# Kernel tuning notes

Hardware: AMD Instinct MI355X
Metric: run time of the kernel (lower is better)

Reference implementation:

```python
import jax, jax.numpy as jnp
import numpy as np

WS = 8          # window size
HEADS = 3       # num_heads
DIM = 48        # channels


def _rel_pos_log(ws):
    # log-spaced relative coordinates, (N, N, 2) with N = ws*ws
    coords = jnp.stack(jnp.meshgrid(jnp.arange(ws), jnp.arange(ws), indexing='ij'))  # (2, ws, ws)
    cf = coords.reshape(2, -1)                                  # (2, N)
    rel = (cf[:, :, None] - cf[:, None, :]).transpose(1, 2, 0)  # (N, N, 2)
    rel = rel.astype(jnp.float32)
    return jnp.sign(rel) * jnp.log1p(jnp.abs(rel))


def setup_inputs() -> dict:
    key = jax.random.key(0)
    ks = jax.random.split(key, 11)
    s = 0.05  # keep pre-softmax logits in a sane range
    return {
        'X': jax.random.normal(ks[0], (2, DIM, 512, 512), jnp.float32),
        'v_w': jax.random.normal(ks[1], (DIM, DIM), jnp.float32) * s,
        'v_b': jnp.zeros((DIM,), jnp.float32),
        'qk_w': jax.random.normal(ks[2], (2 * DIM, DIM), jnp.float32) * s,
        'qk_b': jnp.zeros((2 * DIM,), jnp.float32),
        'proj_w': jax.random.normal(ks[3], (DIM, DIM), jnp.float32) * s,
        'proj_b': jnp.zeros((DIM,), jnp.float32),
        'meta1_w': jax.random.normal(ks[4], (256, 2), jnp.float32) * s,
        'meta1_b': jnp.zeros((256,), jnp.float32),
        'meta2_w': jax.random.normal(ks[5], (HEADS, 256), jnp.float32) * s,
        'meta2_b': jnp.zeros((HEADS,), jnp.float32),
    }


def _conv1x1(x, w, b):
    # x: [B, Cin, H, W], w: [Cout, Cin], b: [Cout]
    return jnp.einsum('oc,bchw->bohw', w, x) + b[None, :, None, None]


def reference(X, v_w, v_b, qk_w, qk_b, proj_w, proj_b,
              meta1_w, meta1_b, meta2_w, meta2_b):
    B, C, H, W = X.shape
    hd = C // HEADS
    scale = hd ** -0.5
    N = WS * WS

    V = _conv1x1(X, v_w, v_b)              # [B, C, H, W]
    QK = _conv1x1(X, qk_w, qk_b)           # [B, 2C, H, W]
    QKV = jnp.concatenate([QK, V], axis=1)  # [B, 3C, H, W]

    # window partition (shift=0, H/W multiples of WS -> no padding)
    nh, nw = H // WS, W // WS
    x = QKV.transpose(0, 2, 3, 1)                           # [B, H, W, 3C]
    x = x.reshape(B, nh, WS, nw, WS, 3 * C)
    x = x.transpose(0, 1, 3, 2, 4, 5).reshape(B * nh * nw, N, 3 * C)

    qkv = x.reshape(-1, N, 3, HEADS, hd).transpose(2, 0, 3, 1, 4)  # [3, B_, h, N, d]
    q, k, v = qkv[0], qkv[1], qkv[2]

    attn = jnp.einsum('bhnd,bhmd->bhnm', q * scale, k)       # [B_, h, N, N]

    # MLP relative position bias
    rel = _rel_pos_log(WS)                                   # [N, N, 2]
    hidden = jax.nn.relu(rel @ meta1_w.T + meta1_b)          # [N, N, 256]
    bias = (hidden @ meta2_w.T + meta2_b).transpose(2, 0, 1)  # [h, N, N]

    attn = jax.nn.softmax(attn + bias[None], axis=-1)
    out = jnp.einsum('bhnm,bhmd->bhnd', attn, v)             # [B_, h, N, d]
    out = out.transpose(0, 2, 1, 3).reshape(B * nh * nw, N, C)

    # window reverse
    out = out.reshape(B, nh, nw, WS, WS, C)
    out = out.transpose(0, 1, 3, 2, 4, 5).reshape(B, H, W, C)
    out = out.transpose(0, 3, 1, 2)                          # [B, C, H, W]

    return _conv1x1(out, proj_w, proj_b)
```

## Files before the change

### kernel.cpp

```cpp
#include <hip/hip_runtime.h>
#include <math.h>


typedef _Float16 f16x4 __attribute__((ext_vector_type(4)));
typedef float    f32x4 __attribute__((ext_vector_type(4)));

#define LOG2E 1.44269504f

#define WS_BFRAG 0
#define WS_WFRAG 49152
#define WS_PFRAG 62976
#define WS_QKVB  67584
#define WS_PBIAS 68160

#define XT_S 52
#define K_S  52
#define VD_S 68

__global__ __launch_bounds__(256) void prep_kernel(
    const float* __restrict__ m1w, const float* __restrict__ m1b,
    const float* __restrict__ m2w, const float* __restrict__ m2b,
    const float* __restrict__ qk_w, const float* __restrict__ v_w,
    const float* __restrict__ proj_w,
    const float* __restrict__ qk_b, const float* __restrict__ v_b,
    const float* __restrict__ proj_b,
    unsigned char* __restrict__ ws)
{
    __shared__ float sm[1536];

    float*     bfrag = (float*)(ws + WS_BFRAG);
    _Float16*  wfrag = (_Float16*)(ws + WS_WFRAG);
    _Float16*  pfrag = (_Float16*)(ws + WS_PFRAG);
    float*     qkvb  = (float*)(ws + WS_QKVB);
    float*     pbias = (float*)(ws + WS_PBIAS);

    const int gid = blockIdx.x * 256 + threadIdx.x;
    if (blockIdx.x < 16) {
        for (int i = threadIdx.x; i < 1536; i += 256) {
            float v;
            if (i < 512)      v = m1w[i];
            else if (i < 768) v = m1b[i - 512];
            else              v = m2w[i - 768];
            sm[i] = v;
        }
        __syncthreads();

        const int n = gid >> 6, m = gid & 63;
        float di = (float)((n >> 3) - (m >> 3));
        float dj = (float)((n & 7) - (m & 7));
        float r0 = copysignf(log1pf(fabsf(di)), di);
        float r1 = copysignf(log1pf(fabsf(dj)), dj);
        float a0 = 0.f, a1 = 0.f, a2 = 0.f;
        #pragma unroll 4
        for (int k = 0; k < 256; ++k) {
            float hv = fmaxf(sm[512 + k] + sm[2*k]*r0 + sm[2*k+1]*r1, 0.f);
            a0 += sm[768 + k]  * hv;
            a1 += sm[1024 + k] * hv;
            a2 += sm[1280 + k] * hv;
        }
        const int tm = m >> 4, quad = (m >> 2) & 3, r = m & 3, tn = n >> 4;
        const int ln = quad*16 + (n & 15);
        const int base = ((tm*4 + tn)*64 + ln)*4 + r;
        bfrag[(0*16*64)*4  + base] = (a0 + m2b[0]) * LOG2E;
        bfrag[(16*64)*4    + base] = (a1 + m2b[1]) * LOG2E;
        bfrag[(32*64)*4    + base] = (a2 + m2b[2]) * LOG2E;
    } else if (gid < 4096 + 6912) {
        const int idx = gid - 4096;
        const int j = idx & 3, l = (idx >> 2) & 63, f = idx >> 8;
        const int ks = f % 3, mt = f / 3;
        const int row = mt*16 + (l & 15), col = ks*16 + ((l >> 4) << 2) + j;
        const float wv = (row < 96) ? qk_w[row*48 + col] : v_w[(row-96)*48 + col];
        wfrag[idx] = (_Float16)wv;
    } else if (gid < 11008 + 2304) {
        const int idx = gid - 11008;
        const int j = idx & 3, l = (idx >> 2) & 63, f = idx >> 8;
        const int ks = f % 3, mt = f / 3;
        const int row = mt*16 + (l & 15), col = ks*16 + ((l >> 4) << 2) + j;
        pfrag[idx] = (_Float16)proj_w[row*48 + col];
    } else if (gid < 13312 + 144) {
        const int c = gid - 13312;
        qkvb[c] = (c < 96) ? qk_b[c] : v_b[c - 96];
    } else if (gid < 13456 + 48) {
        pbias[gid - 13456] = proj_b[gid - 13456];
    }
}

__global__ __launch_bounds__(256, 8) void win_attn_kernel(
    const float* __restrict__ X, const unsigned char* __restrict__ ws,
    float* __restrict__ out, int nblk)
{
    __shared__ _Float16 smem[9920];
    _Float16* sXO = smem;
    _Float16* sK  = smem + 64*XT_S;
    _Float16* sVd = smem + 64*XT_S + 64*K_S;

    const float* bfrag = (const float*)(ws + WS_BFRAG);
    const f16x4* wfrag = (const f16x4*)(ws + WS_WFRAG);
    const f16x4* pfrag = (const f16x4*)(ws + WS_PFRAG);
    const float* qkvb  = (const float*)(ws + WS_QKVB);
    const float* pbias = (const float*)(ws + WS_PBIAS);

    const int tid  = threadIdx.x;
    const int wave = tid >> 6, lane = tid & 63;
    const int lq   = lane >> 4, lm = lane & 15;

    const int blk = blockIdx.x;
    const int wid = (blk & 7) * (nblk >> 3) + (blk >> 3);
    const int batch = wid >> 12;
    const int wh = (wid >> 6) & 63, ww = wid & 63;
    const int h0 = wh << 3, w0 = ww << 3;

    const float* Xb = X + ((size_t)batch * 48 << 18);

    {
        const int tok = lane;
        const size_t pix = (size_t)(h0 + (tok >> 3)) * 512 + (w0 + (tok & 7));
        #pragma unroll
        for (int k = 0; k < 12; ++k) {
            const int c = wave + (k << 2);
            sXO[tok*XT_S + c] = (_Float16)Xb[((size_t)c << 18) + pix];
        }
    }
    __syncthreads();

    f16x4 qf[3];
    {
        f16x4 bx[3];
        #pragma unroll
        for (int ks = 0; ks < 3; ++ks)
            bx[ks] = *(const f16x4*)&sXO[(wave*16 + lm)*XT_S + ks*16 + lq*4];

        const int tok = wave*16 + lm;
        #pragma unroll
        for (int mt = 0; mt < 9; ++mt) {
            f32x4 acc = *(const f32x4*)&qkvb[mt*16 + lq*4];
            #pragma unroll
            for (int ks = 0; ks < 3; ++ks)
                acc = __builtin_amdgcn_mfma_f32_16x16x16f16(
                          wfrag[(mt*3+ks)*64 + lane], bx[ks], acc, 0, 0, 0);
            if (mt < 3) {
                #pragma unroll
                for (int r = 0; r < 4; ++r)
                    qf[mt][r] = (_Float16)(acc[r] * (0.25f * LOG2E));
            } else if (mt < 6) {
                f16x4 hv;
                #pragma unroll
                for (int r = 0; r < 4; ++r) hv[r] = (_Float16)acc[r];
                *(f16x4*)&sK[tok*K_S + (mt-3)*16 + lq*4] = hv;
            } else {
                #pragma unroll
                for (int r = 0; r < 4; ++r)
                    sVd[((mt-6)*16 + lq*4 + r)*VD_S + tok] = (_Float16)acc[r];
            }
        }
    }
    __syncthreads();

    const int tn = wave;
    const f32x4* bf = (const f32x4*)bfrag;
    #pragma unroll
    for (int h = 0; h < 3; ++h) {
        f16x4 ak[4];
        #pragma unroll
        for (int tm = 0; tm < 4; ++tm)
            ak[tm] = *(const f16x4*)&sK[(tm*16 + lm)*K_S + h*16 + lq*4];
        f32x4 s[4];
        #pragma unroll
        for (int tm = 0; tm < 4; ++tm)
            s[tm] = __builtin_amdgcn_mfma_f32_16x16x16f16(
                        ak[tm], qf[h], bf[(h*16 + tm*4 + tn)*64 + lane], 0, 0, 0);

        float sum = 0.f;
        #pragma unroll
        for (int tm = 0; tm < 4; ++tm)
            #pragma unroll
            for (int r = 0; r < 4; ++r) {
                float e = __builtin_amdgcn_exp2f(s[tm][r]);
                s[tm][r] = e; sum += e;
            }
        sum += __shfl_xor(sum, 16);
        sum += __shfl_xor(sum, 32);
        const float rinv = __builtin_amdgcn_rcpf(sum);

        f32x4 o = {0.f, 0.f, 0.f, 0.f};
        #pragma unroll
        for (int tm = 0; tm < 4; ++tm) {
            f16x4 av = *(const f16x4*)&sVd[(h*16 + lm)*VD_S + tm*16 + lq*4];
            f16x4 pf;
            pf[0] = (_Float16)s[tm][0];
            pf[1] = (_Float16)s[tm][1];
            pf[2] = (_Float16)s[tm][2];
            pf[3] = (_Float16)s[tm][3];
            o = __builtin_amdgcn_mfma_f32_16x16x16f16(av, pf, o, 0, 0, 0);
        }
        f16x4 hv;
        #pragma unroll
        for (int r = 0; r < 4; ++r) hv[r] = (_Float16)(o[r] * rinv);
        *(f16x4*)&sXO[(tn*16 + lm)*XT_S + h*16 + lq*4] = hv;
    }

    {
        f16x4 bo[3];
        #pragma unroll
        for (int ks = 0; ks < 3; ++ks)
            bo[ks] = *(const f16x4*)&sXO[(wave*16 + lm)*XT_S + ks*16 + lq*4];

        const int tok = wave*16 + lm;
        float* ob = out + ((size_t)batch * 48 << 18);
        const size_t pix = (size_t)(h0 + (tok >> 3)) * 512 + (w0 + (tok & 7));
        #pragma unroll
        for (int mt = 0; mt < 3; ++mt) {
            f32x4 acc = *(const f32x4*)&pbias[mt*16 + lq*4];
            #pragma unroll
            for (int ks = 0; ks < 3; ++ks)
                acc = __builtin_amdgcn_mfma_f32_16x16x16f16(
                          pfrag[(mt*3+ks)*64 + lane], bo[ks], acc, 0, 0, 0);
            #pragma unroll
            for (int r = 0; r < 4; ++r)
                ob[((size_t)(mt*16 + lq*4 + r) << 18) + pix] = acc[r];
        }
    }
}

extern "C" void kernel_launch(void* const* d_in, const int* in_sizes, int n_in,
                              void* d_out, int out_size, void* d_ws, size_t ws_size,
                              hipStream_t stream) {
    (void)n_in; (void)out_size; (void)ws_size;
    const float* X      = (const float*)d_in[0];
    const float* v_w    = (const float*)d_in[1];
    const float* v_b    = (const float*)d_in[2];
    const float* qk_w   = (const float*)d_in[3];
    const float* qk_b   = (const float*)d_in[4];
    const float* proj_w = (const float*)d_in[5];
    const float* proj_b = (const float*)d_in[6];
    const float* m1w    = (const float*)d_in[7];
    const float* m1b    = (const float*)d_in[8];
    const float* m2w    = (const float*)d_in[9];
    const float* m2b    = (const float*)d_in[10];
    float* out = (float*)d_out;
    unsigned char* ws = (unsigned char*)d_ws;

    const int B = in_sizes[0] / (48 * 512 * 512);
    const int nblk = B * 64 * 64;

    hipLaunchKernelGGL(prep_kernel, dim3(53), dim3(256), 0, stream,
                       m1w, m1b, m2w, m2b, qk_w, v_w, proj_w, qk_b, v_b, proj_b, ws);
    hipLaunchKernelGGL(win_attn_kernel, dim3(nblk), dim3(256), 0, stream,
                       X, ws, out, nblk);
}
```

Before: 284.0 us.

## Process two horizontally adjacent windows per 512-thread block with per-head waves

Each block now handles two neighbouring 8x8 windows (a 16-wide pixel strip) with 8 waves. Global loads and stores cover 16 contiguous pixels per row for better coalescing. Attention work is split so each of three waves per window owns one head, with Q staged in shared memory. One wave per window idles during attention, and the block uses more LDS and adds an extra barrier, which may reduce occupancy.

```diff
diff --git a/kernel.cpp b/kernel.cpp
--- a/kernel.cpp
+++ b/kernel.cpp
@@ -14,7 +14,7 @@
 #define WS_PBIAS 68160
 
 #define XT_S 52
-#define K_S  52
+#define T_S  100
 #define VD_S 68
 
 __global__ __launch_bounds__(256) void prep_kernel(
@@ -85,14 +85,14 @@
     }
 }
 
-__global__ __launch_bounds__(256, 8) void win_attn_kernel(
+__global__ __launch_bounds__(512, 6) void win_attn_kernel(
     const float* __restrict__ X, const unsigned char* __restrict__ ws,
     float* __restrict__ out, int nblk)
 {
-    __shared__ _Float16 smem[9920];
-    _Float16* sXO = smem;
-    _Float16* sK  = smem + 64*XT_S;
-    _Float16* sVd = smem + 64*XT_S + 64*K_S;
+    __shared__ _Float16 smem[25984];
+    _Float16* sA = smem;
+    _Float16* sT = smem + 128*XT_S;
+    _Float16* sV = smem + 128*XT_S + 128*T_S;
 
     const float* bfrag = (const float*)(ws + WS_BFRAG);
     const f16x4* wfrag = (const f16x4*)(ws + WS_WFRAG);
@@ -101,36 +101,45 @@
     const float* pbias = (const float*)(ws + WS_PBIAS);
 
     const int tid  = threadIdx.x;
-    const int wave = tid >> 6, lane = tid & 63;
+    const int wv   = tid >> 6, lane = tid & 63;
     const int lq   = lane >> 4, lm = lane & 15;
 
     const int blk = blockIdx.x;
     const int wid = (blk & 7) * (nblk >> 3) + (blk >> 3);
-    const int batch = wid >> 12;
-    const int wh = (wid >> 6) & 63, ww = wid & 63;
-    const int h0 = wh << 3, w0 = ww << 3;
+    const int batch = wid >> 11;
+    const int wh = (wid >> 5) & 63, wp = wid & 31;
+    const int h0 = wh << 3, w0 = wp << 4;
 
     const float* Xb = X + ((size_t)batch * 48 << 18);
 
     {
-        const int tok = lane;
-        const size_t pix = (size_t)(h0 + (tok >> 3)) * 512 + (w0 + (tok & 7));
+        const int seg = lane >> 4, col = lane & 15;
+        float xv[12];
         #pragma unroll
         for (int k = 0; k < 12; ++k) {
-            const int c = wave + (k << 2);
-            sXO[tok*XT_S + c] = (_Float16)Xb[((size_t)c << 18) + pix];
+            const int c   = wv + ((k >> 1) << 3);
+            const int row = ((k & 1) << 2) + seg;
+            xv[k] = Xb[((size_t)c << 18) + (size_t)(h0 + row) * 512 + (w0 + col)];
+        }
+        #pragma unroll
+        for (int k = 0; k < 12; ++k) {
+            const int c    = wv + ((k >> 1) << 3);
+            const int row  = ((k & 1) << 2) + seg;
+            const int gtok = ((col >> 3) << 6) + (row << 3) + (col & 7);
+            sA[gtok*XT_S + c] = (_Float16)xv[k];
         }
     }
     __syncthreads();
 
-    f16x4 qf[3];
     {
         f16x4 bx[3];
         #pragma unroll
         for (int ks = 0; ks < 3; ++ks)
-            bx[ks] = *(const f16x4*)&sXO[(wave*16 + lm)*XT_S + ks*16 + lq*4];
-
-        const int tok = wave*16 + lm;
+            bx[ks] = *(const f16x4*)&sA[(wv*16 + lm)*XT_S + ks*16 + lq*4];
+
+        const int gtok = wv*16 + lm;
+        const int tok  = (wv & 3)*16 + lm;
+        const int winb = (wv >> 2) * 48 * VD_S;
         #pragma unroll
         for (int mt = 0; mt < 9; ++mt) {
             f32x4 acc = *(const f32x4*)&qkvb[mt*16 + lq*4];
@@ -139,75 +148,89 @@
                 acc = __builtin_amdgcn_mfma_f32_16x16x16f16(
                           wfrag[(mt*3+ks)*64 + lane], bx[ks], acc, 0, 0, 0);
             if (mt < 3) {
-                #pragma unroll
-                for (int r = 0; r < 4; ++r)
-                    qf[mt][r] = (_Float16)(acc[r] * (0.25f * LOG2E));
+                f16x4 hv;
+                #pragma unroll
+                for (int r = 0; r < 4; ++r) hv[r] = (_Float16)(acc[r] * (0.25f*LOG2E));
+                *(f16x4*)&sT[gtok*T_S + mt*16 + lq*4] = hv;
             } else if (mt < 6) {
                 f16x4 hv;
                 #pragma unroll
                 for (int r = 0; r < 4; ++r) hv[r] = (_Float16)acc[r];
-                *(f16x4*)&sK[tok*K_S + (mt-3)*16 + lq*4] = hv;
+                *(f16x4*)&sT[gtok*T_S + mt*16 + lq*4] = hv;
             } else {
                 #pragma unroll
                 for (int r = 0; r < 4; ++r)
-                    sVd[((mt-6)*16 + lq*4 + r)*VD_S + tok] = (_Float16)acc[r];
+                    sV[winb + ((mt-6)*16 + lq*4 + r)*VD_S + tok] = (_Float16)acc[r];
             }
         }
     }
     __syncthreads();
 
-    const int tn = wave;
-    const f32x4* bf = (const f32x4*)bfrag;
-    #pragma unroll
-    for (int h = 0; h < 3; ++h) {
-        f16x4 ak[4];
+    if ((wv & 3) < 3) {
+        const int h = wv & 3, base = (wv >> 2) << 6;
+        const int winb = (wv >> 2) * 48 * VD_S;
+        f16x4 ak[4], bq[4];
+        #pragma unroll
+        for (int t = 0; t < 4; ++t) {
+            ak[t] = *(const f16x4*)&sT[(base + t*16 + lm)*T_S + 48 + h*16 + lq*4];
+            bq[t] = *(const f16x4*)&sT[(base + t*16 + lm)*T_S + h*16 + lq*4];
+        }
+        f32x4 s[4][4];
+        const f32x4* bf = (const f32x4*)bfrag + (size_t)h*16*64;
         #pragma unroll
         for (int tm = 0; tm < 4; ++tm)
-            ak[tm] = *(const f16x4*)&sK[(tm*16 + lm)*K_S + h*16 + lq*4];
-        f32x4 s[4];
+            #pragma unroll
+            for (int tn = 0; tn < 4; ++tn)
+                s[tm][tn] = __builtin_amdgcn_mfma_f32_16x16x16f16(
+                                ak[tm], bq[tn], bf[(tm*4 + tn)*64 + lane], 0, 0, 0);
+        float rinv[4];
+        #pragma unroll
+        for (int tn = 0; tn < 4; ++tn) {
+            float sum = 0.f;
+            #pragma unroll
+            for (int tm = 0; tm < 4; ++tm)
+                #pragma unroll
+                for (int r = 0; r < 4; ++r) {
+                    float e = __builtin_amdgcn_exp2f(s[tm][tn][r]);
+                    s[tm][tn][r] = e; sum += e;
+                }
+            sum += __shfl_xor(sum, 16);
+            sum += __shfl_xor(sum, 32);
+            rinv[tn] = __builtin_amdgcn_rcpf(sum);
+        }
+        f16x4 av[4];
         #pragma unroll
         for (int tm = 0; tm < 4; ++tm)
-            s[tm] = __builtin_amdgcn_mfma_f32_16x16x16f16(
-                        ak[tm], qf[h], bf[(h*16 + tm*4 + tn)*64 + lane], 0, 0, 0);
-
-        float sum = 0.f;
-        #pragma unroll
-        for (int tm = 0; tm < 4; ++tm)
-            #pragma unroll
-            for (int r = 0; r < 4; ++r) {
-                float e = __builtin_amdgcn_exp2f(s[tm][r]);
-                s[tm][r] = e; sum += e;
+            av[tm] = *(const f16x4*)&sV[winb + (h*16 + lm)*VD_S + tm*16 + lq*4];
+        #pragma unroll
+        for (int tn = 0; tn < 4; ++tn) {
+            f32x4 o = {0.f, 0.f, 0.f, 0.f};
+            #pragma unroll
+            for (int tm = 0; tm < 4; ++tm) {
+                f16x4 pf;
+                pf[0] = (_Float16)s[tm][tn][0];
+                pf[1] = (_Float16)s[tm][tn][1];
+                pf[2] = (_Float16)s[tm][tn][2];
+                pf[3] = (_Float16)s[tm][tn][3];
+                o = __builtin_amdgcn_mfma_f32_16x16x16f16(av[tm], pf, o, 0, 0, 0);
             }
-        sum += __shfl_xor(sum, 16);
-        sum += __shfl_xor(sum, 32);
-        const float rinv = __builtin_amdgcn_rcpf(sum);
-
-        f32x4 o = {0.f, 0.f, 0.f, 0.f};
-        #pragma unroll
-        for (int tm = 0; tm < 4; ++tm) {
-            f16x4 av = *(const f16x4*)&sVd[(h*16 + lm)*VD_S + tm*16 + lq*4];
-            f16x4 pf;
-            pf[0] = (_Float16)s[tm][0];
-            pf[1] = (_Float16)s[tm][1];
-            pf[2] = (_Float16)s[tm][2];
-            pf[3] = (_Float16)s[tm][3];
-            o = __builtin_amdgcn_mfma_f32_16x16x16f16(av, pf, o, 0, 0, 0);
-        }
-        f16x4 hv;
-        #pragma unroll
-        for (int r = 0; r < 4; ++r) hv[r] = (_Float16)(o[r] * rinv);
-        *(f16x4*)&sXO[(tn*16 + lm)*XT_S + h*16 + lq*4] = hv;
-    }
+            f16x4 hv;
+            #pragma unroll
+            for (int r = 0; r < 4; ++r) hv[r] = (_Float16)(o[r] * rinv[tn]);
+            *(f16x4*)&sA[(base + tn*16 + lm)*XT_S + h*16 + lq*4] = hv;
+        }
+    }
+    __syncthreads();
 
     {
+        const int gt4 = ((lm >> 3) << 6) + (wv << 3) + (lm & 7);
         f16x4 bo[3];
         #pragma unroll
         for (int ks = 0; ks < 3; ++ks)
-            bo[ks] = *(const f16x4*)&sXO[(wave*16 + lm)*XT_S + ks*16 + lq*4];
-
-        const int tok = wave*16 + lm;
+            bo[ks] = *(const f16x4*)&sA[gt4*XT_S + ks*16 + lq*4];
+
         float* ob = out + ((size_t)batch * 48 << 18);
-        const size_t pix = (size_t)(h0 + (tok >> 3)) * 512 + (w0 + (tok & 7));
+        const size_t pixr = (size_t)(h0 + wv) * 512 + w0 + lm;
         #pragma unroll
         for (int mt = 0; mt < 3; ++mt) {
             f32x4 acc = *(const f32x4*)&pbias[mt*16 + lq*4];
@@ -217,7 +240,7 @@
                           pfrag[(mt*3+ks)*64 + lane], bo[ks], acc, 0, 0, 0);
             #pragma unroll
             for (int r = 0; r < 4; ++r)
-                ob[((size_t)(mt*16 + lq*4 + r) << 18) + pix] = acc[r];
+                ob[((size_t)(mt*16 + lq*4 + r) << 18) + pixr] = acc[r];
         }
     }
 }
@@ -241,10 +264,10 @@
     unsigned char* ws = (unsigned char*)d_ws;
 
     const int B = in_sizes[0] / (48 * 512 * 512);
-    const int nblk = B * 64 * 64;
+    const int nblk = B * 64 * 32;
 
     hipLaunchKernelGGL(prep_kernel, dim3(53), dim3(256), 0, stream,
                        m1w, m1b, m2w, m2b, qk_w, v_w, proj_w, qk_b, v_b, proj_b, ws);
-    hipLaunchKernelGGL(win_attn_kernel, dim3(nblk), dim3(256), 0, stream,
+    hipLaunchKernelGGL(win_attn_kernel, dim3(nblk), dim3(512), 0, stream,
                        X, ws, out, nblk);
 }
```

Result: slower. 312.6 us (+10.0%).
